# Kernel tuning notes

Hardware: AMD Instinct MI355X
Metric: run time of the kernel (lower is better)

The kernel has to match this reference:

```python
import jax, jax.numpy as jnp
import numpy as np

IN_FEATURES = 4096
OUT_FEATURES = 16384


def setup_inputs() -> dict:
    key = jax.random.key(0)
    k_x, k_w = jax.random.split(key)
    x = jax.random.normal(k_x, (8192, IN_FEATURES), dtype=jnp.float32)
    weight = jax.random.normal(k_w, (OUT_FEATURES, IN_FEATURES), dtype=jnp.float32)
    return {"x": x, "weight": weight}


def ternary_quantize(weight):
    # scale = mean(|W|) clamped; quantize to {-1,0,1}*scale
    scale = jnp.maximum(jnp.mean(jnp.abs(weight)), 1e-8)
    q = jnp.round(jnp.clip(weight / scale, -1.0, 1.0)) * scale
    return q


def reference(x, weight):
    qw = ternary_quantize(weight)  # [out, in]
    # F.linear: x @ W^T
    return jnp.einsum('ti,oi->to', x, qw)
```

## Files before the change

### kernel.cpp

```cpp
#include <hip/hip_runtime.h>
#include <hip/hip_bf16.h>
#include <stdint.h>

typedef __attribute__((ext_vector_type(4))) int i32x4;

#define M_DIM 8192
#define K_DIM 4096
#define N_DIM 16384
#define NELEM_W ((long)N_DIM * (long)K_DIM)
#define NELEM_X ((long)M_DIM * (long)K_DIM)


__device__ __forceinline__ void g2l16(const void* g, void* l) {
  __builtin_amdgcn_global_load_lds(
      (const __attribute__((address_space(1))) unsigned int*)g,
      (__attribute__((address_space(3))) unsigned int*)l, 16, 0, 0);
}


__global__ void reduce_absw(const float4* __restrict__ w4, double* __restrict__ partials, int n4) {
  const int tid = threadIdx.x;
  double s = 0.0;
  const int stride = gridDim.x * blockDim.x;
  for (int i = blockIdx.x * blockDim.x + tid; i < n4; i += stride) {
    float4 v = w4[i];
    s += (double)fabsf(v.x);
    s += (double)fabsf(v.y);
    s += (double)fabsf(v.z);
    s += (double)fabsf(v.w);
  }
  __shared__ double sd[256];
  sd[tid] = s;
  __syncthreads();
  for (int off = 128; off > 0; off >>= 1) {
    if (tid < off) sd[tid] += sd[tid + off];
    __syncthreads();
  }
  if (tid == 0) partials[blockIdx.x] = sd[0];
}

__global__ void finalize_scale(const double* __restrict__ partials, float* __restrict__ sp) {
  const int tid = threadIdx.x;
  double s = 0.0;
#pragma unroll
  for (int j = 0; j < 8; ++j) s += partials[tid * 8 + j];
  __shared__ double sd[256];
  sd[tid] = s;
  __syncthreads();
  for (int off = 128; off > 0; off >>= 1) {
    if (tid < off) sd[tid] += sd[tid + off];
    __syncthreads();
  }
  if (tid == 0) {
    double mean = sd[0] / (double)NELEM_W;
    float sc = (float)mean;
    if (sc < 1e-8f) sc = 1e-8f;
    sp[0] = sc;
  }
}


__global__ void quant_w_i8(const float4* __restrict__ w4, char* __restrict__ q,
                           const float* __restrict__ sp, int n4) {
  const float sc = sp[0];
  const int stride = gridDim.x * blockDim.x;
  for (int i = blockIdx.x * blockDim.x + threadIdx.x; i < n4; i += stride) {
    float4 v = w4[i];
    char4 o;
    o.x = (char)rintf(fminf(fmaxf(v.x / sc, -1.f), 1.f));
    o.y = (char)rintf(fminf(fmaxf(v.y / sc, -1.f), 1.f));
    o.z = (char)rintf(fminf(fmaxf(v.z / sc, -1.f), 1.f));
    o.w = (char)rintf(fminf(fmaxf(v.w / sc, -1.f), 1.f));
    *(char4*)(q + (long)i * 4) = o;
  }
}


__global__ __launch_bounds__(256)
void quant_x_i8(const float* __restrict__ x, char* __restrict__ xq,
                float* __restrict__ s_row) {
  const int row = blockIdx.x;
  const int tid = threadIdx.x;
  const float4* xr = (const float4*)(x + (long)row * K_DIM);
  float4 v[4];
  float m = 0.f;
#pragma unroll
  for (int k = 0; k < 4; ++k) {
    v[k] = xr[tid + 256 * k];
    m = fmaxf(m, fmaxf(fmaxf(fabsf(v[k].x), fabsf(v[k].y)),
                       fmaxf(fabsf(v[k].z), fabsf(v[k].w))));
  }
  __shared__ float red[256];
  red[tid] = m;
  __syncthreads();
  for (int off = 128; off > 0; off >>= 1) {
    if (tid < off) red[tid] = fmaxf(red[tid], red[tid + off]);
    __syncthreads();
  }
  const float mx = red[0];
  const float inv = (mx > 0.f) ? (127.f / mx) : 0.f;
  if (tid == 0) s_row[row] = (mx > 0.f) ? (mx / 127.f) : 0.f;
  char4* out = (char4*)(xq + (long)row * K_DIM);
#pragma unroll
  for (int k = 0; k < 4; ++k) {
    char4 o;
    o.x = (char)fminf(fmaxf(rintf(v[k].x * inv), -127.f), 127.f);
    o.y = (char)fminf(fmaxf(rintf(v[k].y * inv), -127.f), 127.f);
    o.z = (char)fminf(fmaxf(rintf(v[k].z * inv), -127.f), 127.f);
    o.w = (char)fminf(fmaxf(rintf(v[k].w * inv), -127.f), 127.f);
    out[tid + 256 * k] = o;
  }
}


template<int MP, int NP, int AH>
__device__ __forceinline__ void mb(i32x4 (&acc)[8][4], const i32x4 (&a)[8], const i32x4 (&b)[8]) {
#pragma unroll
  for (int dm = 0; dm < 2; ++dm)
#pragma unroll
    for (int dn = 0; dn < 2; ++dn)
#pragma unroll
      for (int ks = 0; ks < 2; ++ks)
        acc[MP * 2 + dm][NP * 2 + dn] = __builtin_amdgcn_mfma_i32_16x16x64_i8(
            a[AH + dm * 2 + ks], b[NP * 4 + dn * 2 + ks], acc[MP * 2 + dm][NP * 2 + dn], 0, 0, 0);
}

#define FENCE asm volatile("" ::: "memory")
#define BAR do { FENCE; __builtin_amdgcn_s_barrier(); FENCE; } while (0)
#define VMW0 asm volatile("s_waitcnt vmcnt(0)" ::: "memory")
#define PRIO1 __builtin_amdgcn_s_setprio(1)
#define PRIO0 __builtin_amdgcn_s_setprio(0)

#define STG_A(bb, h, kt) do { \
    const char* g_ = Ac + aG + (unsigned)(h) * 524288u + (unsigned)(kt) * 128u; \
    char* l_ = lds + (unsigned)(bb) * 32768u + (unsigned)(h) * 16384u + ldsT; \
    g2l16(g_, l_); g2l16(g_ + 262144u, l_ + 8192u); \
  } while (0)
#define STG_B(bb, h, kt) do { \
    const char* g_ = Bc + bG + (unsigned)(h) * 524288u + (unsigned)(kt) * 128u; \
    char* l_ = lds + 65536u + (unsigned)(bb) * 32768u + (unsigned)(h) * 16384u + ldsT; \
    g2l16(g_, l_); g2l16(g_ + 262144u, l_ + 8192u); \
  } while (0)

#define LDA_(d, bb, m, ks) d = *(const i32x4*)(lds + Abase##bb + (unsigned)(m) * 2048u + frk + coff##ks)
#define LDB_(d, bb, n, ks) d = *(const i32x4*)(lds + Bbase##bb + (unsigned)(n) * 2048u + frk + coff##ks)

#define RD_A(AH, bb, mp) do { \
    LDA_(a[(AH) + 0], bb, 2 * (mp) + 0, 0); LDA_(a[(AH) + 1], bb, 2 * (mp) + 0, 1); \
    LDA_(a[(AH) + 2], bb, 2 * (mp) + 1, 0); LDA_(a[(AH) + 3], bb, 2 * (mp) + 1, 1); \
  } while (0)
#define RD_B(bb, np) do { \
    LDB_(b[4 * (np) + 0], bb, 2 * (np) + 0, 0); LDB_(b[4 * (np) + 1], bb, 2 * (np) + 0, 1); \
    LDB_(b[4 * (np) + 2], bb, 2 * (np) + 1, 0); LDB_(b[4 * (np) + 3], bb, 2 * (np) + 1, 1); \
  } while (0)

#define TILE(bb, obb, kt1, DO_STG) do { \
    if (DO_STG) { STG_A(obb, 0, kt1); STG_A(obb, 1, kt1); STG_B(obb, 0, kt1); STG_B(obb, 1, kt1); } \
    RD_A(0, bb, 0); RD_B(bb, 0); \
    PRIO1; mb<0, 0, 0>(acc, a, b); PRIO0; \
    RD_A(4, bb, 1); RD_B(bb, 1); \
    PRIO1; mb<0, 1, 0>(acc, a, b); PRIO0; \
    RD_A(0, bb, 2); \
    PRIO1; mb<1, 1, 4>(acc, a, b); PRIO0; \
    PRIO1; mb<1, 0, 4>(acc, a, b); PRIO0; \
    RD_A(4, bb, 3); \
    PRIO1; mb<2, 0, 0>(acc, a, b); PRIO0; \
    PRIO1; mb<2, 1, 0>(acc, a, b); PRIO0; \
    PRIO1; mb<3, 1, 4>(acc, a, b); PRIO0; \
    PRIO1; mb<3, 0, 4>(acc, a, b); PRIO0; \
  } while (0)

__global__ __launch_bounds__(512, 2)
void gemm_i8(const char* __restrict__ A, const char* __restrict__ B,
             float* __restrict__ C, const float* __restrict__ sp,
             const float* __restrict__ s_row) {
  extern __shared__ char lds[];

  const int tid = threadIdx.x;
  const int wave = tid >> 6, lane = tid & 63;
  const int fr = lane & 15, fq = lane >> 4;
  const int wr = wave >> 2;
  const int wc = wave & 3;

  int wgid = blockIdx.x;
  wgid = (wgid & 7) * ((int)gridDim.x >> 3) + (wgid >> 3);
  const int bm = wgid >> 6;
  const int bn = wgid & 63;

  const int r0 = tid >> 3;
  const int pslot = tid & 7;
  const int lslot = pslot ^ (r0 & 7);
  const unsigned aG = (unsigned)(bm * 256 + r0) * (unsigned)K_DIM + (unsigned)lslot * 16u;
  const unsigned bG = (unsigned)(bn * 256 + r0) * (unsigned)K_DIM + (unsigned)lslot * 16u;
  const unsigned ldsT = (unsigned)tid * 16u;
  const char* Ac = A;
  const char* Bc = B;

  const unsigned axor = (unsigned)(fr & 7) << 4;
  const unsigned coff0 = ((unsigned)(fq * 16)) ^ axor;
  const unsigned coff1 = ((unsigned)(64 + fq * 16)) ^ axor;
  const unsigned frk = (unsigned)fr * 128u;
  const unsigned Abase0 = (unsigned)(wr * 16384);
  const unsigned Abase1 = (unsigned)(32768 + wr * 16384);
  const unsigned Bhalf = (unsigned)(65536 + (wc >> 1) * 16384 + (wc & 1) * 8192);
  const unsigned Bbase0 = Bhalf;
  const unsigned Bbase1 = Bhalf + 32768u;

  i32x4 acc[8][4] = {};
  i32x4 a[8], b[8];

  STG_A(0, 0, 0); STG_A(0, 1, 0); STG_B(0, 0, 0); STG_B(0, 1, 0);
  VMW0;
  BAR;

#pragma unroll 1
  for (int i = 0; i < 15; ++i) {
    TILE(0, 1, 2 * i + 1, true);
    VMW0; BAR;
    TILE(1, 0, 2 * i + 2, true);
    VMW0; BAR;
  }
  TILE(0, 1, 31, true);
  VMW0; BAR;
  TILE(1, 0, 0, false);

  const float sw = sp[0];
  const int crow0 = bm * 256 + wr * 128 + fq * 4;
  const int ccol0 = bn * 256 + wc * 64 + fr;
#pragma unroll
  for (int m = 0; m < 8; ++m) {
#pragma unroll
    for (int j = 0; j < 4; ++j) {
      const int row = crow0 + m * 16 + j;
      const float sc = s_row[row] * sw;
#pragma unroll
      for (int n = 0; n < 4; ++n) {
        C[(long)row * N_DIM + (ccol0 + n * 16)] = (float)acc[m][n][j] * sc;
      }
    }
  }
}


typedef __hip_bfloat16 bf16;
typedef __attribute__((ext_vector_type(8))) short short8;
typedef __attribute__((ext_vector_type(4))) float f32x4;

__device__ __forceinline__ unsigned short f2bf(float f) {
  unsigned int u = __float_as_uint(f);
  u += 0x7FFFu + ((u >> 16) & 1u);
  return (unsigned short)(u >> 16);
}

__global__ __launch_bounds__(256)
void gemm_fly(const float* __restrict__ X, const float* __restrict__ W,
              float* __restrict__ C, const float* __restrict__ sp) {
  __shared__ alignas(16) bf16 As[128 * 32];
  __shared__ alignas(16) bf16 Bs[128 * 32];

  const int tid = threadIdx.x;
  const int wave = tid >> 6;
  const int lane = tid & 63;

  int wgid = blockIdx.x;
  wgid = (wgid & 7) * ((int)gridDim.x >> 3) + (wgid >> 3);
  const int nbn = N_DIM / 128;
  const int bm = wgid / nbn;
  const int bn = wgid % nbn;

  const float sc = sp[0];

  const int wr = (wave >> 1) * 64;
  const int wc = (wave & 1) * 64;
  const int fr = lane & 15;
  const int fq = lane >> 4;
  const char* AsB = (const char*)As;
  const char* BsB = (const char*)Bs;
  const unsigned aoff = (unsigned)((wr + fr) * 64 + fq * 16);
  const unsigned boff = (unsigned)((wc + fr) * 64 + fq * 16);

  f32x4 acc[4][4] = {};

  for (int kt = 0; kt < K_DIM; kt += 32) {
#pragma unroll
    for (int r = 0; r < 4; ++r) {
      int e = r * 1024 + tid * 4;
      int row = e >> 5;
      int k4 = e & 31;
      float4 xv = *(const float4*)(X + (long)(bm * 128 + row) * K_DIM + kt + k4);
      ushort4 xb;
      xb.x = f2bf(xv.x); xb.y = f2bf(xv.y); xb.z = f2bf(xv.z); xb.w = f2bf(xv.w);
      *(ushort4*)(As + e) = xb;
      float4 wv = *(const float4*)(W + (long)(bn * 128 + row) * K_DIM + kt + k4);
      ushort4 wb;
      wb.x = f2bf(rintf(fminf(fmaxf(wv.x / sc, -1.f), 1.f)));
      wb.y = f2bf(rintf(fminf(fmaxf(wv.y / sc, -1.f), 1.f)));
      wb.z = f2bf(rintf(fminf(fmaxf(wv.z / sc, -1.f), 1.f)));
      wb.w = f2bf(rintf(fminf(fmaxf(wv.w / sc, -1.f), 1.f)));
      *(ushort4*)(Bs + e) = wb;
    }
    __syncthreads();

    short8 a[4], b[4];
#pragma unroll
    for (int m = 0; m < 4; ++m)
      a[m] = *(const short8*)(AsB + aoff + m * (16 * 64));
#pragma unroll
    for (int n = 0; n < 4; ++n)
      b[n] = *(const short8*)(BsB + boff + n * (16 * 64));
#pragma unroll
    for (int m = 0; m < 4; ++m)
#pragma unroll
      for (int n = 0; n < 4; ++n)
        acc[m][n] = __builtin_amdgcn_mfma_f32_16x16x32_bf16(a[m], b[n], acc[m][n], 0, 0, 0);

    __syncthreads();
  }

  const long crow0 = (long)(bm * 128 + wr + fq * 4);
  const int ccol0 = bn * 128 + wc + fr;
#pragma unroll
  for (int m = 0; m < 4; ++m)
#pragma unroll
    for (int n = 0; n < 4; ++n)
#pragma unroll
      for (int j = 0; j < 4; ++j) {
        long row = crow0 + (long)(m * 16 + j);
        int col = ccol0 + n * 16;
        C[row * N_DIM + col] = acc[m][n][j] * sc;
      }
}


extern "C" void kernel_launch(void* const* d_in, const int* in_sizes, int n_in,
                              void* d_out, int out_size, void* d_ws, size_t ws_size,
                              hipStream_t stream) {
  const float* x = (const float*)d_in[0];
  const float* w = (const float*)d_in[1];
  float* out = (float*)d_out;

  char* ws = (char*)d_ws;
  double* partials = (double*)ws;
  float* sp = (float*)(ws + 16384);
  const size_t SROW_OFF = 32768;
  const size_t WQ_OFF = SROW_OFF + 32768;
  const size_t XQ_OFF = WQ_OFF + (size_t)NELEM_W;
  const size_t NEEDED = XQ_OFF + (size_t)NELEM_X;

  reduce_absw<<<2048, 256, 0, stream>>>((const float4*)w, partials, (int)(NELEM_W / 4));
  finalize_scale<<<1, 256, 0, stream>>>(partials, sp);

  if (ws_size >= NEEDED) {
    float* s_row = (float*)(ws + SROW_OFF);
    char* wq = ws + WQ_OFF;
    char* xq = ws + XQ_OFF;
    quant_w_i8<<<2048, 256, 0, stream>>>((const float4*)w, wq, sp, (int)(NELEM_W / 4));
    quant_x_i8<<<M_DIM, 256, 0, stream>>>(x, xq, s_row);

    static const int lds_bytes = 131072;
    (void)hipFuncSetAttribute((const void*)gemm_i8,
                              hipFuncAttributeMaxDynamicSharedMemorySize, lds_bytes);
    const int grid = (M_DIM / 256) * (N_DIM / 256);
    gemm_i8<<<grid, 512, lds_bytes, stream>>>(xq, wq, out, sp, s_row);
  } else {
    const int grid = (M_DIM / 128) * (N_DIM / 128);
    gemm_fly<<<grid, 256, 0, stream>>>(x, w, out, sp);
  }
}
```

Measured before the change: 696.7 us.

## Pack ternary weights to 2 bits and unpack in-register inside int8 GEMM

Weights are now quantized into a 2-bit packed layout, a quarter of the int8 size, in a pre-swizzled order. The GEMM stages the packed B tile into a much smaller LDS region and expands it to int8 with v_perm lookups before the MFMAs. The wave tiling also changes from 2x4 to 4x2 to fit the new B reads. This cuts weight-side global traffic and LDS use, allowing more occupancy, but adds ALU unpack work inside the MFMA loop.

```diff
diff --git a/kernel.cpp b/kernel.cpp
--- a/kernel.cpp
+++ b/kernel.cpp
@@ -60,19 +60,31 @@
 }
 
 
-__global__ void quant_w_i8(const float4* __restrict__ w4, char* __restrict__ q,
-                           const float* __restrict__ sp, int n4) {
+__global__ __launch_bounds__(256)
+void quant_w_pack(const float* __restrict__ w, unsigned int* __restrict__ q,
+                  const float* __restrict__ sp) {
   const float sc = sp[0];
-  const int stride = gridDim.x * blockDim.x;
-  for (int i = blockIdx.x * blockDim.x + threadIdx.x; i < n4; i += stride) {
-    float4 v = w4[i];
-    char4 o;
-    o.x = (char)rintf(fminf(fmaxf(v.x / sc, -1.f), 1.f));
-    o.y = (char)rintf(fminf(fmaxf(v.y / sc, -1.f), 1.f));
-    o.z = (char)rintf(fminf(fmaxf(v.z / sc, -1.f), 1.f));
-    o.w = (char)rintf(fminf(fmaxf(v.w / sc, -1.f), 1.f));
-    *(char4*)(q + (long)i * 4) = o;
-  }
+  const int idx = blockIdx.x * 256 + threadIdx.x;
+  const int n = idx >> 8;
+  const int r = idx & 255;
+  const int kt = r >> 3;
+  const int kq = (r >> 1) & 3;
+  const int ks = r & 1;
+  const int k0 = kt * 128 + ks * 64 + kq * 16;
+  const float4* src = (const float4*)(w + (long)n * K_DIM + k0);
+  unsigned int d = 0;
+#pragma unroll
+  for (int j = 0; j < 4; ++j) {
+    float4 v = src[j];
+    int c0 = (int)rintf(fminf(fmaxf(v.x / sc, -1.f), 1.f)) + 1;
+    int c1 = (int)rintf(fminf(fmaxf(v.y / sc, -1.f), 1.f)) + 1;
+    int c2 = (int)rintf(fminf(fmaxf(v.z / sc, -1.f), 1.f)) + 1;
+    int c3 = (int)rintf(fminf(fmaxf(v.w / sc, -1.f), 1.f)) + 1;
+    d |= ((unsigned)c0 << (2 * (j * 4 + 0))) | ((unsigned)c1 << (2 * (j * 4 + 1)))
+       | ((unsigned)c2 << (2 * (j * 4 + 2))) | ((unsigned)c3 << (2 * (j * 4 + 3)));
+  }
+  const int sl = (kq + (n >> 2)) & 3;
+  q[(n * 1024 + kt * 32 + sl * 8 + ks * 4) >> 2] = d;
 }
 
 
@@ -113,61 +125,85 @@
 }
 
 
-template<int MP, int NP, int AH>
-__device__ __forceinline__ void mb(i32x4 (&acc)[8][4], const i32x4 (&a)[8], const i32x4 (&b)[8]) {
-#pragma unroll
-  for (int dm = 0; dm < 2; ++dm)
-#pragma unroll
-    for (int dn = 0; dn < 2; ++dn)
-#pragma unroll
-      for (int ks = 0; ks < 2; ++ks)
-        acc[MP * 2 + dm][NP * 2 + dn] = __builtin_amdgcn_mfma_i32_16x16x64_i8(
-            a[AH + dm * 2 + ks], b[NP * 4 + dn * 2 + ks], acc[MP * 2 + dm][NP * 2 + dn], 0, 0, 0);
-}
-
 #define FENCE asm volatile("" ::: "memory")
 #define BAR do { FENCE; __builtin_amdgcn_s_barrier(); FENCE; } while (0)
 #define VMW0 asm volatile("s_waitcnt vmcnt(0)" ::: "memory")
 #define PRIO1 __builtin_amdgcn_s_setprio(1)
 #define PRIO0 __builtin_amdgcn_s_setprio(0)
 
-#define STG_A(bb, h, kt) do { \
+__device__ __forceinline__ int unpk_dword(unsigned int v, int q, unsigned int lut) {
+  unsigned int x = (v >> (8 * q)) & 0xFFu;
+  unsigned int sel = ((x & 0x3Fu) * 0x41041u) & 0x00030303u;
+  sel |= (x >> 6) << 24;
+  int out;
+  asm("v_perm_b32 %0, %1, %2, %3" : "=v"(out) : "v"(lut), "v"(lut), "v"(sel));
+  return out;
+}
+
+__device__ __forceinline__ i32x4 unpk_op(unsigned int v, unsigned int lut) {
+  i32x4 r;
+  r[0] = unpk_dword(v, 0, lut);
+  r[1] = unpk_dword(v, 1, lut);
+  r[2] = unpk_dword(v, 2, lut);
+  r[3] = unpk_dword(v, 3, lut);
+  return r;
+}
+
+#define STG_A(ob, h, kt) do { \
     const char* g_ = Ac + aG + (unsigned)(h) * 524288u + (unsigned)(kt) * 128u; \
-    char* l_ = lds + (unsigned)(bb) * 32768u + (unsigned)(h) * 16384u + ldsT; \
+    char* l_ = lds + (unsigned)(ob) * 32768u + (unsigned)(h) * 16384u + ldsT; \
     g2l16(g_, l_); g2l16(g_ + 262144u, l_ + 8192u); \
   } while (0)
-#define STG_B(bb, h, kt) do { \
-    const char* g_ = Bc + bG + (unsigned)(h) * 524288u + (unsigned)(kt) * 128u; \
-    char* l_ = lds + 65536u + (unsigned)(bb) * 32768u + (unsigned)(h) * 16384u + ldsT; \
-    g2l16(g_, l_); g2l16(g_ + 262144u, l_ + 8192u); \
-  } while (0)
-
-#define LDA_(d, bb, m, ks) d = *(const i32x4*)(lds + Abase##bb + (unsigned)(m) * 2048u + frk + coff##ks)
-#define LDB_(d, bb, n, ks) d = *(const i32x4*)(lds + Bbase##bb + (unsigned)(n) * 2048u + frk + coff##ks)
-
-#define RD_A(AH, bb, mp) do { \
-    LDA_(a[(AH) + 0], bb, 2 * (mp) + 0, 0); LDA_(a[(AH) + 1], bb, 2 * (mp) + 0, 1); \
-    LDA_(a[(AH) + 2], bb, 2 * (mp) + 1, 0); LDA_(a[(AH) + 3], bb, 2 * (mp) + 1, 1); \
-  } while (0)
-#define RD_B(bb, np) do { \
-    LDB_(b[4 * (np) + 0], bb, 2 * (np) + 0, 0); LDB_(b[4 * (np) + 1], bb, 2 * (np) + 0, 1); \
-    LDB_(b[4 * (np) + 2], bb, 2 * (np) + 1, 0); LDB_(b[4 * (np) + 3], bb, 2 * (np) + 1, 1); \
-  } while (0)
-
-#define TILE(bb, obb, kt1, DO_STG) do { \
-    if (DO_STG) { STG_A(obb, 0, kt1); STG_A(obb, 1, kt1); STG_B(obb, 0, kt1); STG_B(obb, 1, kt1); } \
-    RD_A(0, bb, 0); RD_B(bb, 0); \
-    PRIO1; mb<0, 0, 0>(acc, a, b); PRIO0; \
-    RD_A(4, bb, 1); RD_B(bb, 1); \
-    PRIO1; mb<0, 1, 0>(acc, a, b); PRIO0; \
-    RD_A(0, bb, 2); \
-    PRIO1; mb<1, 1, 4>(acc, a, b); PRIO0; \
-    PRIO1; mb<1, 0, 4>(acc, a, b); PRIO0; \
-    RD_A(4, bb, 3); \
-    PRIO1; mb<2, 0, 0>(acc, a, b); PRIO0; \
-    PRIO1; mb<2, 1, 0>(acc, a, b); PRIO0; \
-    PRIO1; mb<3, 1, 4>(acc, a, b); PRIO0; \
-    PRIO1; mb<3, 0, 4>(acc, a, b); PRIO0; \
+#define STG_B(ob, kt) do { \
+    const char* g_ = Bc + bGp + (unsigned)(kt) * 32u; \
+    char* l_ = lds + 65536u + (unsigned)(ob) * 8192u + ldsT; \
+    g2l16(g_, l_); \
+  } while (0)
+
+#define RD_A(bb, mt) do { \
+    a[(mt) * 2 + 0] = *(const i32x4*)(lds + aR##bb + (unsigned)(mt) * 2048u + coff0); \
+    a[(mt) * 2 + 1] = *(const i32x4*)(lds + aR##bb + (unsigned)(mt) * 2048u + coff1); \
+  } while (0)
+#define RD_B64(par, bb, pp) do { \
+    pk##par[0] = *(const uint2*)(lds + bR##bb + (unsigned)(pp) * 1024u); \
+    pk##par[1] = *(const uint2*)(lds + bR##bb + (unsigned)(pp) * 1024u + 512u); \
+  } while (0)
+#define UNPK(par) do { \
+    bu##par[0] = unpk_op(pk##par[0].x, lut); bu##par[1] = unpk_op(pk##par[0].y, lut); \
+    bu##par[2] = unpk_op(pk##par[1].x, lut); bu##par[3] = unpk_op(pk##par[1].y, lut); \
+  } while (0)
+
+#define MFMA8(NP, MH, BU) do { PRIO1; \
+    _Pragma("unroll") \
+    for (int dm = 0; dm < 2; ++dm) \
+      _Pragma("unroll") \
+      for (int dn = 0; dn < 2; ++dn) \
+        _Pragma("unroll") \
+        for (int ks = 0; ks < 2; ++ks) \
+          acc[(MH) * 2 + dm][(NP) * 2 + dn] = __builtin_amdgcn_mfma_i32_16x16x64_i8( \
+              a[((MH) * 2 + dm) * 2 + ks], BU[dn * 2 + ks], acc[(MH) * 2 + dm][(NP) * 2 + dn], 0, 0, 0); \
+    PRIO0; } while (0)
+
+#define TILE(bb, ob, kt1, DO_STG) do { \
+    if (DO_STG) { STG_A(ob, 0, kt1); STG_A(ob, 1, kt1); STG_B(ob, kt1); } \
+    RD_B64(0, bb, 0); \
+    RD_A(bb, 0); RD_A(bb, 1); \
+    UNPK(0); \
+    RD_B64(1, bb, 1); \
+    RD_A(bb, 2); RD_A(bb, 3); \
+    MFMA8(0, 0, bu0); \
+    UNPK(1); \
+    MFMA8(0, 1, bu0); \
+    RD_B64(0, bb, 2); \
+    MFMA8(1, 0, bu1); \
+    UNPK(0); \
+    MFMA8(1, 1, bu1); \
+    RD_B64(1, bb, 3); \
+    MFMA8(2, 0, bu0); \
+    UNPK(1); \
+    MFMA8(2, 1, bu0); \
+    MFMA8(3, 0, bu1); \
+    MFMA8(3, 1, bu1); \
   } while (0)
 
 __global__ __launch_bounds__(512, 2)
@@ -179,8 +215,8 @@
   const int tid = threadIdx.x;
   const int wave = tid >> 6, lane = tid & 63;
   const int fr = lane & 15, fq = lane >> 4;
-  const int wr = wave >> 2;
-  const int wc = wave & 3;
+  const int wm = wave >> 1;
+  const int wn = wave & 1;
 
   int wgid = blockIdx.x;
   wgid = (wgid & 7) * ((int)gridDim.x >> 3) + (wgid >> 3);
@@ -191,7 +227,7 @@
   const int pslot = tid & 7;
   const int lslot = pslot ^ (r0 & 7);
   const unsigned aG = (unsigned)(bm * 256 + r0) * (unsigned)K_DIM + (unsigned)lslot * 16u;
-  const unsigned bG = (unsigned)(bn * 256 + r0) * (unsigned)K_DIM + (unsigned)lslot * 16u;
+  const unsigned bGp = (unsigned)(bn * 256 + (tid >> 1)) * 1024u + (unsigned)(tid & 1) * 16u;
   const unsigned ldsT = (unsigned)tid * 16u;
   const char* Ac = A;
   const char* Bc = B;
@@ -199,17 +235,20 @@
   const unsigned axor = (unsigned)(fr & 7) << 4;
   const unsigned coff0 = ((unsigned)(fq * 16)) ^ axor;
   const unsigned coff1 = ((unsigned)(64 + fq * 16)) ^ axor;
-  const unsigned frk = (unsigned)fr * 128u;
-  const unsigned Abase0 = (unsigned)(wr * 16384);
-  const unsigned Abase1 = (unsigned)(32768 + wr * 16384);
-  const unsigned Bhalf = (unsigned)(65536 + (wc >> 1) * 16384 + (wc & 1) * 8192);
-  const unsigned Bbase0 = Bhalf;
-  const unsigned Bbase1 = Bhalf + 32768u;
-
-  i32x4 acc[8][4] = {};
-  i32x4 a[8], b[8];
-
-  STG_A(0, 0, 0); STG_A(0, 1, 0); STG_B(0, 0, 0); STG_B(0, 1, 0);
+  const unsigned aR0 = (unsigned)((wm >> 1) * 16384 + (wm & 1) * 8192 + fr * 128);
+  const unsigned aR1 = aR0 + 32768u;
+  const unsigned bslot = (unsigned)(((lane >> 4) + (fr >> 2)) & 3);
+  const unsigned bR0 = 65536u + (unsigned)(wn * 128 + fr) * 32u + bslot * 8u;
+  const unsigned bR1 = bR0 + 8192u;
+
+  const unsigned int lut = 0x000100FFu;
+
+  i32x4 acc[4][8] = {};
+  i32x4 a[8];
+  uint2 pk0[2], pk1[2];
+  i32x4 bu0[4], bu1[4];
+
+  STG_A(0, 0, 0); STG_A(0, 1, 0); STG_B(0, 0);
   VMW0;
   BAR;
 
@@ -225,17 +264,17 @@
   TILE(1, 0, 0, false);
 
   const float sw = sp[0];
-  const int crow0 = bm * 256 + wr * 128 + fq * 4;
-  const int ccol0 = bn * 256 + wc * 64 + fr;
-#pragma unroll
-  for (int m = 0; m < 8; ++m) {
+  const int crow0 = bm * 256 + wm * 64 + fq * 4;
+  const int ccol0 = bn * 256 + wn * 128 + fr;
+#pragma unroll
+  for (int mt = 0; mt < 4; ++mt) {
 #pragma unroll
     for (int j = 0; j < 4; ++j) {
-      const int row = crow0 + m * 16 + j;
-      const float sc = s_row[row] * sw;
-#pragma unroll
-      for (int n = 0; n < 4; ++n) {
-        C[(long)row * N_DIM + (ccol0 + n * 16)] = (float)acc[m][n][j] * sc;
+      const int row = crow0 + mt * 16 + j;
+      const float scl = s_row[row] * sw;
+#pragma unroll
+      for (int nt = 0; nt < 8; ++nt) {
+        C[(long)row * N_DIM + (ccol0 + nt * 16)] = (float)acc[mt][nt][j] * scl;
       }
     }
   }
@@ -344,7 +383,7 @@
   float* sp = (float*)(ws + 16384);
   const size_t SROW_OFF = 32768;
   const size_t WQ_OFF = SROW_OFF + 32768;
-  const size_t XQ_OFF = WQ_OFF + (size_t)NELEM_W;
+  const size_t XQ_OFF = WQ_OFF + (size_t)N_DIM * 1024;
   const size_t NEEDED = XQ_OFF + (size_t)NELEM_X;
 
   reduce_absw<<<2048, 256, 0, stream>>>((const float4*)w, partials, (int)(NELEM_W / 4));
@@ -352,16 +391,16 @@
 
   if (ws_size >= NEEDED) {
     float* s_row = (float*)(ws + SROW_OFF);
-    char* wq = ws + WQ_OFF;
+    unsigned int* wq = (unsigned int*)(ws + WQ_OFF);
     char* xq = ws + XQ_OFF;
-    quant_w_i8<<<2048, 256, 0, stream>>>((const float4*)w, wq, sp, (int)(NELEM_W / 4));
+    quant_w_pack<<<(N_DIM * 256) / 256, 256, 0, stream>>>(w, wq, sp);
     quant_x_i8<<<M_DIM, 256, 0, stream>>>(x, xq, s_row);
 
-    static const int lds_bytes = 131072;
+    static const int lds_bytes = 81920;
     (void)hipFuncSetAttribute((const void*)gemm_i8,
                               hipFuncAttributeMaxDynamicSharedMemorySize, lds_bytes);
     const int grid = (M_DIM / 256) * (N_DIM / 256);
-    gemm_i8<<<grid, 512, lds_bytes, stream>>>(xq, wq, out, sp, s_row);
+    gemm_i8<<<grid, 512, lds_bytes, stream>>>(xq, (const char*)wq, out, sp, s_row);
   } else {
     const int grid = (M_DIM / 128) * (N_DIM / 128);
     gemm_fly<<<grid, 256, 0, stream>>>(x, w, out, sp);
```

Result: slower. 935.9 us (+34.3%).

## Shrink int8 GEMM tile to 128x256 with K-step 64 for higher occupancy

Applied to the files above, without the earlier changes.

Reworks the int8 MFMA GEMM tile from 256x256 with K-step 128 to 128x256 with K-step 64. This cuts LDS use from 128KB to 48KB and the accumulators from 8x4 to 4x4, and raises the launch-bounds occupancy target from 2 to 4 workgroups per CU. The LDS swizzle and the interleaved read/MFMA schedule are simplified to straight loops. The aim is better latency hiding through more resident waves, at the cost of less operand reuse per load and twice as many barriers per K.

```diff
diff --git a/kernel.cpp b/kernel.cpp
--- a/kernel.cpp
+++ b/kernel.cpp
@@ -113,64 +113,37 @@
 }
 
 
-template<int MP, int NP, int AH>
-__device__ __forceinline__ void mb(i32x4 (&acc)[8][4], const i32x4 (&a)[8], const i32x4 (&b)[8]) {
-#pragma unroll
-  for (int dm = 0; dm < 2; ++dm)
-#pragma unroll
-    for (int dn = 0; dn < 2; ++dn)
-#pragma unroll
-      for (int ks = 0; ks < 2; ++ks)
-        acc[MP * 2 + dm][NP * 2 + dn] = __builtin_amdgcn_mfma_i32_16x16x64_i8(
-            a[AH + dm * 2 + ks], b[NP * 4 + dn * 2 + ks], acc[MP * 2 + dm][NP * 2 + dn], 0, 0, 0);
-}
-
 #define FENCE asm volatile("" ::: "memory")
 #define BAR do { FENCE; __builtin_amdgcn_s_barrier(); FENCE; } while (0)
 #define VMW0 asm volatile("s_waitcnt vmcnt(0)" ::: "memory")
 #define PRIO1 __builtin_amdgcn_s_setprio(1)
 #define PRIO0 __builtin_amdgcn_s_setprio(0)
 
-#define STG_A(bb, h, kt) do { \
-    const char* g_ = Ac + aG + (unsigned)(h) * 524288u + (unsigned)(kt) * 128u; \
-    char* l_ = lds + (unsigned)(bb) * 32768u + (unsigned)(h) * 16384u + ldsT; \
-    g2l16(g_, l_); g2l16(g_ + 262144u, l_ + 8192u); \
+#define STG(ob, kt) do { \
+    g2l16(Ac + aG + (unsigned)(kt) * 64u, lds + (unsigned)(ob) * 8192u + ldsT); \
+    char* bl_ = lds + 16384u + (unsigned)(ob) * 16384u + ldsT; \
+    g2l16(Bc + bG + (unsigned)(kt) * 64u, bl_); \
+    g2l16(Bc + bG + 524288u + (unsigned)(kt) * 64u, bl_ + 8192u); \
   } while (0)
-#define STG_B(bb, h, kt) do { \
-    const char* g_ = Bc + bG + (unsigned)(h) * 524288u + (unsigned)(kt) * 128u; \
-    char* l_ = lds + 65536u + (unsigned)(bb) * 32768u + (unsigned)(h) * 16384u + ldsT; \
-    g2l16(g_, l_); g2l16(g_ + 262144u, l_ + 8192u); \
+
+#define TILE(bb, ob, kt1, DO_STG) do { \
+    if (DO_STG) STG(ob, kt1); \
+    _Pragma("unroll") \
+    for (int mt = 0; mt < 4; ++mt) \
+      a[mt] = *(const i32x4*)(lds + (unsigned)(bb) * 8192u + aRd + (unsigned)mt * 1024u); \
+    _Pragma("unroll") \
+    for (int nt = 0; nt < 4; ++nt) \
+      b[nt] = *(const i32x4*)(lds + 16384u + (unsigned)(bb) * 16384u + bRd + (unsigned)nt * 1024u); \
+    PRIO1; \
+    _Pragma("unroll") \
+    for (int mt = 0; mt < 4; ++mt) \
+      _Pragma("unroll") \
+      for (int nt = 0; nt < 4; ++nt) \
+        acc[mt][nt] = __builtin_amdgcn_mfma_i32_16x16x64_i8(a[mt], b[nt], acc[mt][nt], 0, 0, 0); \
+    PRIO0; \
   } while (0)
 
-#define LDA_(d, bb, m, ks) d = *(const i32x4*)(lds + Abase##bb + (unsigned)(m) * 2048u + frk + coff##ks)
-#define LDB_(d, bb, n, ks) d = *(const i32x4*)(lds + Bbase##bb + (unsigned)(n) * 2048u + frk + coff##ks)
-
-#define RD_A(AH, bb, mp) do { \
-    LDA_(a[(AH) + 0], bb, 2 * (mp) + 0, 0); LDA_(a[(AH) + 1], bb, 2 * (mp) + 0, 1); \
-    LDA_(a[(AH) + 2], bb, 2 * (mp) + 1, 0); LDA_(a[(AH) + 3], bb, 2 * (mp) + 1, 1); \
-  } while (0)
-#define RD_B(bb, np) do { \
-    LDB_(b[4 * (np) + 0], bb, 2 * (np) + 0, 0); LDB_(b[4 * (np) + 1], bb, 2 * (np) + 0, 1); \
-    LDB_(b[4 * (np) + 2], bb, 2 * (np) + 1, 0); LDB_(b[4 * (np) + 3], bb, 2 * (np) + 1, 1); \
-  } while (0)
-
-#define TILE(bb, obb, kt1, DO_STG) do { \
-    if (DO_STG) { STG_A(obb, 0, kt1); STG_A(obb, 1, kt1); STG_B(obb, 0, kt1); STG_B(obb, 1, kt1); } \
-    RD_A(0, bb, 0); RD_B(bb, 0); \
-    PRIO1; mb<0, 0, 0>(acc, a, b); PRIO0; \
-    RD_A(4, bb, 1); RD_B(bb, 1); \
-    PRIO1; mb<0, 1, 0>(acc, a, b); PRIO0; \
-    RD_A(0, bb, 2); \
-    PRIO1; mb<1, 1, 4>(acc, a, b); PRIO0; \
-    PRIO1; mb<1, 0, 4>(acc, a, b); PRIO0; \
-    RD_A(4, bb, 3); \
-    PRIO1; mb<2, 0, 0>(acc, a, b); PRIO0; \
-    PRIO1; mb<2, 1, 0>(acc, a, b); PRIO0; \
-    PRIO1; mb<3, 1, 4>(acc, a, b); PRIO0; \
-    PRIO1; mb<3, 0, 4>(acc, a, b); PRIO0; \
-  } while (0)
-
-__global__ __launch_bounds__(512, 2)
+__global__ __launch_bounds__(512, 4)
 void gemm_i8(const char* __restrict__ A, const char* __restrict__ B,
              float* __restrict__ C, const float* __restrict__ sp,
              const float* __restrict__ s_row) {
@@ -179,63 +152,56 @@
   const int tid = threadIdx.x;
   const int wave = tid >> 6, lane = tid & 63;
   const int fr = lane & 15, fq = lane >> 4;
-  const int wr = wave >> 2;
-  const int wc = wave & 3;
+  const int wm = wave >> 2;
+  const int wn = wave & 3;
 
   int wgid = blockIdx.x;
   wgid = (wgid & 7) * ((int)gridDim.x >> 3) + (wgid >> 3);
   const int bm = wgid >> 6;
   const int bn = wgid & 63;
 
-  const int r0 = tid >> 3;
-  const int pslot = tid & 7;
-  const int lslot = pslot ^ (r0 & 7);
-  const unsigned aG = (unsigned)(bm * 256 + r0) * (unsigned)K_DIM + (unsigned)lslot * 16u;
+  const int r0 = tid >> 2;
+  const int lslot = (tid & 3) ^ (r0 & 3);
+  const unsigned aG = (unsigned)(bm * 128 + r0) * (unsigned)K_DIM + (unsigned)lslot * 16u;
   const unsigned bG = (unsigned)(bn * 256 + r0) * (unsigned)K_DIM + (unsigned)lslot * 16u;
   const unsigned ldsT = (unsigned)tid * 16u;
   const char* Ac = A;
   const char* Bc = B;
 
-  const unsigned axor = (unsigned)(fr & 7) << 4;
-  const unsigned coff0 = ((unsigned)(fq * 16)) ^ axor;
-  const unsigned coff1 = ((unsigned)(64 + fq * 16)) ^ axor;
-  const unsigned frk = (unsigned)fr * 128u;
-  const unsigned Abase0 = (unsigned)(wr * 16384);
-  const unsigned Abase1 = (unsigned)(32768 + wr * 16384);
-  const unsigned Bhalf = (unsigned)(65536 + (wc >> 1) * 16384 + (wc & 1) * 8192);
-  const unsigned Bbase0 = Bhalf;
-  const unsigned Bbase1 = Bhalf + 32768u;
-
-  i32x4 acc[8][4] = {};
-  i32x4 a[8], b[8];
-
-  STG_A(0, 0, 0); STG_A(0, 1, 0); STG_B(0, 0, 0); STG_B(0, 1, 0);
+  const unsigned sswz = ((unsigned)(fq ^ (fr & 3))) << 4;
+  const unsigned aRd = (unsigned)(wm * 64 + fr) * 64u + sswz;
+  const unsigned bRd = (unsigned)(wn * 64 + fr) * 64u + sswz;
+
+  i32x4 acc[4][4] = {};
+  i32x4 a[4], b[4];
+
+  STG(0, 0);
   VMW0;
   BAR;
 
 #pragma unroll 1
-  for (int i = 0; i < 15; ++i) {
+  for (int i = 0; i < 31; ++i) {
     TILE(0, 1, 2 * i + 1, true);
     VMW0; BAR;
     TILE(1, 0, 2 * i + 2, true);
     VMW0; BAR;
   }
-  TILE(0, 1, 31, true);
+  TILE(0, 1, 63, true);
   VMW0; BAR;
   TILE(1, 0, 0, false);
 
   const float sw = sp[0];
-  const int crow0 = bm * 256 + wr * 128 + fq * 4;
-  const int ccol0 = bn * 256 + wc * 64 + fr;
-#pragma unroll
-  for (int m = 0; m < 8; ++m) {
+  const int crow0 = bm * 128 + wm * 64 + fq * 4;
+  const int ccol0 = bn * 256 + wn * 64 + fr;
+#pragma unroll
+  for (int mt = 0; mt < 4; ++mt) {
 #pragma unroll
     for (int j = 0; j < 4; ++j) {
-      const int row = crow0 + m * 16 + j;
-      const float sc = s_row[row] * sw;
-#pragma unroll
-      for (int n = 0; n < 4; ++n) {
-        C[(long)row * N_DIM + (ccol0 + n * 16)] = (float)acc[m][n][j] * sc;
+      const int row = crow0 + mt * 16 + j;
+      const float scl = s_row[row] * sw;
+#pragma unroll
+      for (int nt = 0; nt < 4; ++nt) {
+        C[(long)row * N_DIM + (ccol0 + nt * 16)] = (float)acc[mt][nt][j] * scl;
       }
     }
   }
@@ -357,10 +323,10 @@
     quant_w_i8<<<2048, 256, 0, stream>>>((const float4*)w, wq, sp, (int)(NELEM_W / 4));
     quant_x_i8<<<M_DIM, 256, 0, stream>>>(x, xq, s_row);
 
-    static const int lds_bytes = 131072;
+    static const int lds_bytes = 49152;
     (void)hipFuncSetAttribute((const void*)gemm_i8,
                               hipFuncAttributeMaxDynamicSharedMemorySize, lds_bytes);
-    const int grid = (M_DIM / 256) * (N_DIM / 256);
+    const int grid = (M_DIM / 128) * (N_DIM / 256);
     gemm_i8<<<grid, 512, lds_bytes, stream>>>(xq, wq, out, sp, s_row);
   } else {
     const int grid = (M_DIM / 128) * (N_DIM / 128);
```

Result: slower. 867.0 us (+24.4%).
